# Kernel tuning notes

Measured on AMD Instinct MI355X. Metric: run time of the kernel, lower is better.

Reference implementation:

```python
import jax, jax.numpy as jnp
import numpy as np

B, T, KD, QD, AD, VD, W = 16, 4096, 1024, 1024, 512, 1024, 8


def moving_sum(x, back, forward):
    # x: [B, T] -> windowed sum over [t-back, t+forward], matches F.conv1d with ones filter
    xp = jnp.pad(x, ((0, 0), (back, forward)))[:, None, :]
    filt = jnp.ones((1, 1, back + forward + 1), x.dtype)
    y = jax.lax.conv_general_dilated(xp, filt, (1,), 'VALID')
    return y[:, 0, :]


def setup_inputs() -> dict:
    key = jax.random.key(0)
    ks = jax.random.split(key, 16)
    inp = {
        'key': jax.random.normal(ks[0], (B, T, KD), jnp.float32),
        'value': jax.random.normal(ks[1], (B, T, VD), jnp.float32),
        'query': jax.random.normal(ks[2], (B, 1, QD), jnp.float32),
        'noise': jax.random.normal(ks[3], (B, T), jnp.float32),
        'Wk_mono': jax.random.normal(ks[4], (KD, AD), jnp.float32) * (KD ** -0.5),
        'b_mono': jnp.zeros((AD,), jnp.float32),
        'Wq_mono': jax.random.normal(ks[5], (QD, AD), jnp.float32) * (QD ** -0.5),
        'Wk_chunk': jax.random.normal(ks[6], (KD, AD), jnp.float32) * (KD ** -0.5),
        'b_chunk': jnp.zeros((AD,), jnp.float32),
        'Wq_chunk': jax.random.normal(ks[7], (QD, AD), jnp.float32) * (QD ** -0.5),
        'r_mono': jnp.array([-4.0], jnp.float32),
        'r_chunk': jnp.array([-4.0], jnp.float32),
    }
    # weight-normalized v vectors: g = sqrt(1/attn_dim), w = g * v/||v||
    g = (1.0 / AD) ** 0.5
    vm = jax.random.normal(ks[8], (AD,), jnp.float32)
    vc = jax.random.normal(ks[9], (AD,), jnp.float32)
    inp['v_mono'] = g * vm / jnp.linalg.norm(vm)
    inp['v_chunk'] = g * vc / jnp.linalg.norm(vc)
    return inp


def _forward(key, value, query, noise, Wk_mono, b_mono, Wq_mono, v_mono, r_mono,
             Wk_chunk, b_chunk, Wq_chunk, v_chunk, r_chunk):
    bs, kmax = key.shape[0], key.shape[1]
    # aw_prev default: one-hot at position 0
    aw_prev = jnp.zeros((bs, kmax), key.dtype).at[:, 0].set(1.0)

    # monotonic energy: [B, T]
    qm = jnp.einsum('bqd,da->bqa', query, Wq_mono)  # [B,1,A], broadcasts over T
    e_mono = jnp.einsum('bta,a->bt', jnp.tanh(key @ Wk_mono + b_mono + qm), v_mono) + r_mono

    # parallel mode: sigmoid with additive gaussian noise
    p_choose = jax.nn.sigmoid(e_mono + noise)
    # safe_cumprod with the original's exclusive_cumsum (prepends ONES, drops last)
    log1mp = jnp.log(jnp.clip(1.0 - p_choose, 1e-10, 1.0))
    shifted = jnp.concatenate([jnp.ones((bs, 1), key.dtype), log1mp[:, :-1]], axis=1)
    cumprod_1mp = jnp.exp(jnp.cumsum(shifted, axis=1))
    aw = p_choose * cumprod_1mp * jnp.cumsum(
        aw_prev / jnp.clip(cumprod_1mp, 1e-10, 1.0), axis=1)

    # chunk energy
    qc = jnp.einsum('bqd,da->bqa', query, Wq_chunk)
    e_chunk = jnp.einsum('bta,a->bt', jnp.tanh(key @ Wk_chunk + b_chunk + qc), v_chunk) + r_chunk

    # efficient chunkwise attention
    u = e_chunk - jnp.max(e_chunk, axis=1, keepdims=True)
    softmax_exp = jnp.maximum(jnp.exp(u), 1e-5)
    denom = moving_sum(softmax_exp, back=W - 1, forward=0)
    beta = softmax_exp * moving_sum(aw / denom, back=0, forward=W - 1)

    cv = jnp.einsum('bt,btd->bd', beta, value)[:, None, :]  # [B,1,VD]
    return cv, aw[..., None]


def reference(key, value, query, noise, Wk_mono, b_mono, Wq_mono, v_mono, r_mono,
              Wk_chunk, b_chunk, Wq_chunk, v_chunk, r_chunk):
    return _forward(key, value, query, noise, Wk_mono, b_mono, Wq_mono, v_mono, r_mono,
                    Wk_chunk, b_chunk, Wq_chunk, v_chunk, r_chunk)
```

## Files before the change

### kernel.cpp

```cpp
#include <hip/hip_runtime.h>
#include <hip/hip_bf16.h>
#include <math.h>

#define B_   16
#define T_   4096
#define KD_  1024
#define AD_  512
#define VD_  1024

typedef float f32x4 __attribute__((ext_vector_type(4)));
typedef short s16x8 __attribute__((ext_vector_type(8)));

static __device__ __forceinline__ short f2bf(float f) {
    __hip_bfloat16 h = __float2bfloat16(f);
    return __builtin_bit_cast(short, h);
}

static __device__ __forceinline__ float fast_tanh(float x) {
    x = fminf(fmaxf(x, -15.f), 15.f);
    float e = __expf(2.f * x);
    return (e - 1.f) / (e + 1.f);
}

static __device__ __forceinline__ void gload16(const void* g, void* l) {
    __builtin_amdgcn_global_load_lds(
        (const __attribute__((address_space(1))) void*)(g),
        (__attribute__((address_space(3))) void*)(l), 16, 0, 0);
}


__global__ __launch_bounds__(256) void prep_kernel(
    const float* __restrict__ key, short* __restrict__ keyB,
    const float* __restrict__ Wk_mono, const float* __restrict__ Wk_chunk,
    short* __restrict__ WkTB,
    const float* __restrict__ query,
    const float* __restrict__ Wq_mono, const float* __restrict__ b_mono,
    const float* __restrict__ Wq_chunk, const float* __restrict__ b_chunk,
    float* __restrict__ qb,
    float* __restrict__ e_ws, float* __restrict__ outzero) {
    int bid = blockIdx.x;
    int tid = threadIdx.x;

    if (bid < 4096) {
        const size_t nchunk = (size_t)B_ * T_ * KD_ / 8;
        size_t stride = (size_t)4096 * 256;
        for (size_t g = (size_t)bid * 256 + tid; g < nchunk; g += stride) {
            const float* p = key + g * 8;
            f32x4 f0 = *reinterpret_cast<const f32x4*>(p);
            f32x4 f1 = *reinterpret_cast<const f32x4*>(p + 4);
            s16x8 h;
            h[0] = f2bf(f0[0]); h[1] = f2bf(f0[1]); h[2] = f2bf(f0[2]); h[3] = f2bf(f0[3]);
            h[4] = f2bf(f1[0]); h[5] = f2bf(f1[1]); h[6] = f2bf(f1[2]); h[7] = f2bf(f1[3]);
            size_t m = g >> 7;
            int kc = (int)(g & 127);
            size_t mt = m >> 8;
            int r = (int)(m & 255);
            int kt = kc >> 2;
            int sub = kc & 3;
            int c = (r << 2) | (sub ^ ((r >> 1) & 3));
            *reinterpret_cast<s16x8*>(keyB + (((mt * 32 + kt) * 1024 + c) << 3)) = h;
        }
    } else if (bid < 5120) {
        __shared__ float tile[32][33];
        int wbid = bid - 4096;
        int n0 = (wbid & 31) * 32;
        int k0 = (wbid >> 5) * 32;
        int tx = tid & 31;
        int ty = tid >> 5;
        const float* src;
        int nloc;
        if (n0 < 512) { src = Wk_mono;  nloc = n0; }
        else          { src = Wk_chunk; nloc = n0 - 512; }
#pragma unroll
        for (int i = 0; i < 4; ++i) {
            int k = ty + i * 8;
            tile[k][tx] = src[(size_t)(k0 + k) * AD_ + nloc + tx];
        }
        __syncthreads();
        if (tid < 128) {
            int rl = tid >> 2;
            int sub = tid & 3;
            s16x8 h;
#pragma unroll
            for (int j = 0; j < 8; ++j)
                h[j] = f2bf(tile[sub * 8 + j][rl]);
            int n = n0 + rl;
            int nt = n >> 8;
            int rloc = n & 255;
            int kt = k0 >> 5;
            int c = (rloc << 2) | (sub ^ ((rloc >> 1) & 3));
            *reinterpret_cast<s16x8*>(WkTB + (((size_t)(nt * 32 + kt) * 1024 + c) << 3)) = h;
        }
    } else if (bid < 5376) {
        __shared__ float red[4][64];
        int qbid = bid - 5120;
        int b = qbid & 15;
        int mat = (qbid >> 4) & 1;
        int ac = qbid >> 5;
        const float* Wq = mat ? Wq_chunk : Wq_mono;
        const float* bb = mat ? b_chunk : b_mono;
        int al = tid & 63;
        int dg = tid >> 6;
        int a = ac * 64 + al;
        const float* q = query + b * KD_ + dg * 256;
        const float* wp = Wq + (size_t)(dg * 256) * AD_ + a;
        float s = 0.f;
#pragma unroll 4
        for (int d = 0; d < 256; ++d)
            s += q[d] * wp[(size_t)d * AD_];
        red[dg][al] = s;
        __syncthreads();
        if (dg == 0) {
            float t = red[0][al] + red[1][al] + red[2][al] + red[3][al];
            qb[(mat * B_ + b) * AD_ + a] = t + bb[a];
        }
    } else {
        int zbid = bid - 5376;
        f32x4 z = {0.f, 0.f, 0.f, 0.f};
        if (zbid < 128) {
            float* dst = e_ws + (size_t)zbid * 1024 + tid * 4;
            *reinterpret_cast<f32x4*>(dst) = z;
        } else {
            float* dst = outzero + (size_t)(zbid - 128) * 1024 + tid * 4;
            *reinterpret_cast<f32x4*>(dst) = z;
        }
    }
}

__global__ __launch_bounds__(256) void gemm_e_kernel(
    const short* __restrict__ keyB,
    const short* __restrict__ WkTB,
    const float* __restrict__ qb,
    const float* __restrict__ v_mono, const float* __restrict__ v_chunk,
    float* __restrict__ e_ws ) {
    __shared__ short As[2][1024 * 8];
    __shared__ short Bs[2][1024 * 8];
    int tid = threadIdx.x;
    int bid = blockIdx.x;
    int swz = (bid & 7) * 128 + (bid >> 3);
    int mt = swz >> 2;
    int nt = swz & 3;
    int mBase = mt * 256;
    int nBase = nt * 256;
    int lane = tid & 63;
    int wid = tid >> 6;
    int wr = wid >> 1, wc = wid & 1;
    int col16 = lane & 15, g4 = lane >> 4;

    const short* pA[4];
    const short* pB[4];
    int sOff[4];
#pragma unroll
    for (int i = 0; i < 4; ++i) {
        pA[i] = keyB + ((size_t)mt * 32 * 1024 + i * 256 + tid) * 8;
        pB[i] = WkTB + ((size_t)nt * 32 * 1024 + i * 256 + tid) * 8;
        sOff[i] = (i * 256 + wid * 64) * 8;
    }

    int aoff[8], boff[8];
#pragma unroll
    for (int fi = 0; fi < 8; ++fi) {
        int row = wr * 128 + fi * 16 + col16;
        aoff[fi] = (row * 4 + (g4 ^ ((row >> 1) & 3))) * 8;
    }
#pragma unroll
    for (int fj = 0; fj < 8; ++fj) {
        int coln = wc * 128 + fj * 16 + col16;
        boff[fj] = (coln * 4 + (g4 ^ ((coln >> 1) & 3))) * 8;
    }

    f32x4 acc[8][8];
#pragma unroll
    for (int i = 0; i < 8; ++i)
#pragma unroll
        for (int j = 0; j < 8; ++j) acc[i][j] = (f32x4){0.f, 0.f, 0.f, 0.f};

#pragma unroll
    for (int i = 0; i < 4; ++i) {
        gload16(pA[i], &As[0][sOff[i]]);
        gload16(pB[i], &Bs[0][sOff[i]]);
        pA[i] += 8192; pB[i] += 8192;
    }
    __syncthreads();

    int cur = 0;
    for (int kt = 0; kt < 31; ++kt) {
        int nxt = cur ^ 1;
#pragma unroll
        for (int i = 0; i < 4; ++i) {
            gload16(pA[i], &As[nxt][sOff[i]]);
            gload16(pB[i], &Bs[nxt][sOff[i]]);
            pA[i] += 8192; pB[i] += 8192;
        }
        s16x8 bfr[8];
#pragma unroll
        for (int fj = 0; fj < 8; ++fj)
            bfr[fj] = *reinterpret_cast<const s16x8*>(&Bs[cur][boff[fj]]);
#pragma unroll
        for (int fi = 0; fi < 8; ++fi) {
            s16x8 af = *reinterpret_cast<const s16x8*>(&As[cur][aoff[fi]]);
#pragma unroll
            for (int fj = 0; fj < 8; ++fj)
                acc[fi][fj] = __builtin_amdgcn_mfma_f32_16x16x32_bf16(af, bfr[fj], acc[fi][fj], 0, 0, 0);
        }
        __syncthreads();
        cur = nxt;
    }
    {
        s16x8 bfr[8];
#pragma unroll
        for (int fj = 0; fj < 8; ++fj)
            bfr[fj] = *reinterpret_cast<const s16x8*>(&Bs[cur][boff[fj]]);
#pragma unroll
        for (int fi = 0; fi < 8; ++fi) {
            s16x8 af = *reinterpret_cast<const s16x8*>(&As[cur][aoff[fi]]);
#pragma unroll
            for (int fj = 0; fj < 8; ++fj)
                acc[fi][fj] = __builtin_amdgcn_mfma_f32_16x16x32_bf16(af, bfr[fj], acc[fi][fj], 0, 0, 0);
        }
    }

    int bIdx = mBase >> 12;
    int matrix = nBase >> 9;
    int aBase = (nBase & 511) + wc * 128 + col16;
    const float* qbRow = qb + (matrix * B_ + bIdx) * AD_;
    const float* vv = matrix ? v_chunk : v_mono;
    float* eArr = e_ws + matrix * (B_ * T_);
    float qcol[8], vcol[8];
#pragma unroll
    for (int fj = 0; fj < 8; ++fj) {
        int a = aBase + fj * 16;
        qcol[fj] = qbRow[a];
        vcol[fj] = vv[a];
    }
#pragma unroll
    for (int fi = 0; fi < 8; ++fi) {
        float s0 = 0.f, s1 = 0.f, s2 = 0.f, s3 = 0.f;
#pragma unroll
        for (int fj = 0; fj < 8; ++fj) {
            s0 += fast_tanh(acc[fi][fj][0] + qcol[fj]) * vcol[fj];
            s1 += fast_tanh(acc[fi][fj][1] + qcol[fj]) * vcol[fj];
            s2 += fast_tanh(acc[fi][fj][2] + qcol[fj]) * vcol[fj];
            s3 += fast_tanh(acc[fi][fj][3] + qcol[fj]) * vcol[fj];
        }
#pragma unroll
        for (int mask = 1; mask < 16; mask <<= 1) {
            s0 += __shfl_xor(s0, mask, 64);
            s1 += __shfl_xor(s1, mask, 64);
            s2 += __shfl_xor(s2, mask, 64);
            s3 += __shfl_xor(s3, mask, 64);
        }
        if (col16 == 0) {
            int rowB = mBase + wr * 128 + fi * 16 + g4 * 4;
            atomicAdd(&eArr[rowB + 0], s0);
            atomicAdd(&eArr[rowB + 1], s1);
            atomicAdd(&eArr[rowB + 2], s2);
            atomicAdd(&eArr[rowB + 3], s3);
        }
    }
}

__global__ __launch_bounds__(256) void scan_kernel(
    const float* __restrict__ e_ws,
    const float* __restrict__ noise,
    const float* __restrict__ r_mono, const float* __restrict__ r_chunk,
    float* __restrict__ aw_out, float* __restrict__ beta_out) {
    __shared__ float s_aw[T_];
    __shared__ float s_sexp[T_];
    __shared__ float s_ad[T_];
    __shared__ float s_w[4];
    int b = blockIdx.x;
    int tid = threadIdx.x;
    int lane = tid & 63;
    int wid4 = tid >> 6;
    int t0 = tid * 16;
    const float* em = e_ws + b * T_;
    const float* ec = e_ws + B_ * T_ + b * T_;
    const float* nz = noise + b * T_;
    float rm = r_mono[0], rc = r_chunk[0];

    float pv[16], lp[16];
    float run = 0.f;
#pragma unroll
    for (int j = 0; j < 16; ++j) {
        float x = em[t0 + j] + rm + nz[t0 + j];
        float p = 1.f / (1.f + expf(-x));
        pv[j] = p;
        float om = fminf(fmaxf(1.f - p, 1e-10f), 1.f);
        lp[j] = run;
        run += logf(om);
    }
    float x = run;
#pragma unroll
    for (int off = 1; off < 64; off <<= 1) {
        float y = __shfl_up(x, off, 64);
        if (lane >= off) x += y;
    }
    if (lane == 63) s_w[wid4] = x;
    __syncthreads();
    float wbase = 0.f;
#pragma unroll
    for (int i = 0; i < 3; ++i) if (i < wid4) wbase += s_w[i];
    float base = 1.f + (wbase + x - run);
#pragma unroll
    for (int j = 0; j < 16; ++j) {
        float aw = pv[j] * expf(base + lp[j]);
        s_aw[t0 + j] = aw;
        aw_out[b * T_ + t0 + j] = aw;
    }
    float evs[16];
    float lmax = -INFINITY;
#pragma unroll
    for (int j = 0; j < 16; ++j) {
        float v = ec[t0 + j] + rc;
        evs[j] = v;
        lmax = fmaxf(lmax, v);
    }
#pragma unroll
    for (int off = 1; off < 64; off <<= 1)
        lmax = fmaxf(lmax, __shfl_xor(lmax, off, 64));
    __syncthreads();
    if (lane == 0) s_w[wid4] = lmax;
    __syncthreads();
    float mx = fmaxf(fmaxf(s_w[0], s_w[1]), fmaxf(s_w[2], s_w[3]));
#pragma unroll
    for (int j = 0; j < 16; ++j)
        s_sexp[t0 + j] = fmaxf(expf(evs[j] - mx), 1e-5f);
    __syncthreads();
#pragma unroll
    for (int j = 0; j < 16; ++j) {
        int t = t0 + j;
        int lo = t - 7; if (lo < 0) lo = 0;
        float d = 0.f;
        for (int i = lo; i <= t; ++i) d += s_sexp[i];
        s_ad[t] = s_aw[t] / d;
    }
    __syncthreads();
#pragma unroll
    for (int j = 0; j < 16; ++j) {
        int t = t0 + j;
        int hi = t + 7; if (hi > T_ - 1) hi = T_ - 1;
        float m2 = 0.f;
        for (int i = t; i <= hi; ++i) m2 += s_ad[i];
        beta_out[b * T_ + t] = s_sexp[t] * m2;
    }
}

__global__ __launch_bounds__(256) void cv_kernel(
    const float* __restrict__ value,
    const float* __restrict__ beta,
    float* __restrict__ cv) {
    __shared__ float s_beta[128];
    int b = blockIdx.x;
    int tc = blockIdx.y;
    int tid = threadIdx.x;
    int t0 = tc * 128;
    if (tid < 128) s_beta[tid] = beta[b * T_ + t0 + tid];
    __syncthreads();
    int d0 = tid * 4;
    f32x4 acc = {0.f, 0.f, 0.f, 0.f};
    const float* vp = value + (size_t)(b * T_ + t0) * VD_ + d0;
#pragma unroll 4
    for (int i = 0; i < 128; ++i) {
        f32x4 v = *reinterpret_cast<const f32x4*>(vp + (size_t)i * VD_);
        float bt = s_beta[i];
        acc[0] += bt * v[0];
        acc[1] += bt * v[1];
        acc[2] += bt * v[2];
        acc[3] += bt * v[3];
    }
    atomicAdd(&cv[b * VD_ + d0 + 0], acc[0]);
    atomicAdd(&cv[b * VD_ + d0 + 1], acc[1]);
    atomicAdd(&cv[b * VD_ + d0 + 2], acc[2]);
    atomicAdd(&cv[b * VD_ + d0 + 3], acc[3]);
}

extern "C" void kernel_launch(void* const* d_in, const int* in_sizes, int n_in,
                              void* d_out, int out_size, void* d_ws, size_t ws_size,
                              hipStream_t stream) {
    const float* key      = (const float*)d_in[0];
    const float* value    = (const float*)d_in[1];
    const float* query    = (const float*)d_in[2];
    const float* noise    = (const float*)d_in[3];
    const float* Wk_mono  = (const float*)d_in[4];
    const float* b_mono   = (const float*)d_in[5];
    const float* Wq_mono  = (const float*)d_in[6];
    const float* Wk_chunk = (const float*)d_in[7];
    const float* b_chunk  = (const float*)d_in[8];
    const float* Wq_chunk = (const float*)d_in[9];
    const float* r_mono   = (const float*)d_in[10];
    const float* r_chunk  = (const float*)d_in[11];
    const float* v_mono   = (const float*)d_in[12];
    const float* v_chunk  = (const float*)d_in[13];
    float* out = (float*)d_out;

    char* ws = (char*)d_ws;
    size_t off = 0;
    float* e_ws = (float*)(ws + off); off += 2 * B_ * T_ * sizeof(float);
    float* qb   = (float*)(ws + off); off += 2 * B_ * AD_ * sizeof(float);
    short* WkTB = (short*)(ws + off); off += (size_t)KD_ * KD_ * 2;
    float* beta = (float*)(ws + off); off += B_ * T_ * sizeof(float);
    short* keyB = (short*)(ws + off);

    prep_kernel<<<5520, 256, 0, stream>>>(key, keyB, Wk_mono, Wk_chunk, WkTB,
                                          query, Wq_mono, b_mono, Wq_chunk, b_chunk, qb,
                                          e_ws, out);
    gemm_e_kernel<<<1024, 256, 0, stream>>>(keyB, WkTB, qb, v_mono, v_chunk, e_ws);
    scan_kernel<<<16, 256, 0, stream>>>(e_ws, noise, r_mono, r_chunk, out + B_ * VD_, beta);
    cv_kernel<<<dim3(16, 32), 256, 0, stream>>>(value, beta, out);
}
```

Before: 406.1 us.

## Triple-buffer GEMM LDS tiles with partial vmcnt waits instead of full syncs

The energy GEMM's shared-memory staging moves from double to triple buffering. Loads are issued two k-tiles ahead, and each iteration waits only for the oldest tile's loads using s_waitcnt vmcnt(8) plus a raw barrier, instead of a full __syncthreads. The aim is to hide global load latency behind the MFMA work. The cost is 50% more LDS (96KB), launch bounds pinned to one block per CU, and reliance on the exact count of outstanding vector memory ops for correctness.

New measurement: 402.0 us. About the same (-1.0%).

```diff
diff --git a/kernel.cpp b/kernel.cpp
--- a/kernel.cpp
+++ b/kernel.cpp
@@ -127,14 +127,14 @@
     }
 }
 
-__global__ __launch_bounds__(256) void gemm_e_kernel(
+__global__ __launch_bounds__(256, 1) void gemm_e_kernel(
     const short* __restrict__ keyB,
     const short* __restrict__ WkTB,
     const float* __restrict__ qb,
     const float* __restrict__ v_mono, const float* __restrict__ v_chunk,
     float* __restrict__ e_ws ) {
-    __shared__ short As[2][1024 * 8];
-    __shared__ short Bs[2][1024 * 8];
+    __shared__ short As[3][1024 * 8];
+    __shared__ short Bs[3][1024 * 8];
     int tid = threadIdx.x;
     int bid = blockIdx.x;
     int swz = (bid & 7) * 128 + (bid >> 3);
@@ -147,15 +147,19 @@
     int wr = wid >> 1, wc = wid & 1;
     int col16 = lane & 15, g4 = lane >> 4;
 
-    const short* pA[4];
-    const short* pB[4];
+    const short* aT = keyB + ((size_t)mt * 32 * 1024) * 8;
+    const short* bT = WkTB + ((size_t)nt * 32 * 1024) * 8;
     int sOff[4];
 #pragma unroll
-    for (int i = 0; i < 4; ++i) {
-        pA[i] = keyB + ((size_t)mt * 32 * 1024 + i * 256 + tid) * 8;
-        pB[i] = WkTB + ((size_t)nt * 32 * 1024 + i * 256 + tid) * 8;
-        sOff[i] = (i * 256 + wid * 64) * 8;
-    }
+    for (int i = 0; i < 4; ++i) sOff[i] = (i * 256 + wid * 64) * 8;
+
+    auto stage = [&](int buf, int kt) {
+#pragma unroll
+        for (int i = 0; i < 4; ++i) {
+            gload16(aT + ((size_t)kt * 1024 + i * 256 + tid) * 8, &As[buf][sOff[i]]);
+            gload16(bT + ((size_t)kt * 1024 + i * 256 + tid) * 8, &Bs[buf][sOff[i]]);
+        }
+    };
 
     int aoff[8], boff[8];
 #pragma unroll
@@ -175,22 +179,17 @@
 #pragma unroll
         for (int j = 0; j < 8; ++j) acc[i][j] = (f32x4){0.f, 0.f, 0.f, 0.f};
 
-#pragma unroll
-    for (int i = 0; i < 4; ++i) {
-        gload16(pA[i], &As[0][sOff[i]]);
-        gload16(pB[i], &Bs[0][sOff[i]]);
-        pA[i] += 8192; pB[i] += 8192;
-    }
-    __syncthreads();
+    stage(0, 0);
+    stage(1, 1);
 
     int cur = 0;
     for (int kt = 0; kt < 31; ++kt) {
-        int nxt = cur ^ 1;
-#pragma unroll
-        for (int i = 0; i < 4; ++i) {
-            gload16(pA[i], &As[nxt][sOff[i]]);
-            gload16(pB[i], &Bs[nxt][sOff[i]]);
-            pA[i] += 8192; pB[i] += 8192;
+        asm volatile("s_waitcnt vmcnt(8)" ::: "memory");
+        __builtin_amdgcn_s_barrier();
+        asm volatile("" ::: "memory");
+        if (kt < 30) {
+            int pb = cur + 2; if (pb >= 3) pb -= 3;
+            stage(pb, kt + 2);
         }
         s16x8 bfr[8];
 #pragma unroll
@@ -203,10 +202,12 @@
             for (int fj = 0; fj < 8; ++fj)
                 acc[fi][fj] = __builtin_amdgcn_mfma_f32_16x16x32_bf16(af, bfr[fj], acc[fi][fj], 0, 0, 0);
         }
-        __syncthreads();
-        cur = nxt;
+        ++cur; if (cur == 3) cur = 0;
     }
     {
+        asm volatile("s_waitcnt vmcnt(0)" ::: "memory");
+        __builtin_amdgcn_s_barrier();
+        asm volatile("" ::: "memory");
         s16x8 bfr[8];
 #pragma unroll
         for (int fj = 0; fj < 8; ++fj)
```
